# Optimization experiments

Hardware: AMD Instinct MI355X
Metric: run time of the kernel (lower is better)

## Reference

```python
import jax, jax.numpy as jnp
import numpy as np

B, L, E = 8, 2048, 128


def setup_inputs() -> dict:
    key = jax.random.key(0)
    k1, k2, k3, k4 = jax.random.split(key, 4)
    return {
        "Uq": jax.random.normal(k1, (B, L, E), dtype=jnp.float32),
        "Uid": jax.random.normal(k2, (B, L, E), dtype=jnp.float32),
        "mask": jnp.ones((L, L), dtype=jnp.float32),
        "Wc_w": jax.random.normal(k3, (3 * E,), dtype=jnp.float32) * 0.05,
        "Wc_b": jax.random.normal(k4, (), dtype=jnp.float32) * 0.05,
    }


def reference(Uq, Uid, mask, Wc_w, Wc_b):
    # Wc(cat(Uid, Uq, Uid*Uq)) decomposed into three direct projections —
    # exact same math as the Linear over the concatenation, never
    # materializing the [B, L, L, 3E] tensor.
    e = Uq.shape[-1]
    w_id, w_q, w_mul = Wc_w[:e], Wc_w[e:2 * e], Wc_w[2 * e:]
    s_id = jnp.einsum("bie,e->bi", Uid, w_id)          # [B, Lid]
    s_q = jnp.einsum("bje,e->bj", Uq, w_q)             # [B, Lq]
    s_mul = jnp.einsum("bie,bje,e->bij", Uid, Uq, w_mul)  # [B, Lid, Lq]
    S = (s_id[:, :, None] + s_q[:, None, :] + s_mul + Wc_b) * mask
    # S_D2Q = Softmax(dim=0) over the per-example [Lid, Lq] matrix -> axis=1
    P = jax.nn.softmax(S, axis=1)                      # [B, Lid, Lq]
    A_D2Q = jnp.einsum("bij,bje->bie", P, Uq)          # [B, Lid, E]
    M = jnp.einsum("bij,bkj->bik", P, P)               # P @ P^T, [B, Lid, Lid]
    A_Q2D = jnp.einsum("bik,bke->bie", M, Uid)         # [B, Lid, E]
    Vid = jnp.concatenate([Uid, A_D2Q, Uid * A_D2Q, Uid * A_Q2D], axis=-1)
    return Vid  # [B, Lid, 4E]
```

## Files before the change

### kernel.cpp

```cpp
#include <hip/hip_runtime.h>

#define L 2048
#define E 128
#define NB 8

typedef float f32x4 __attribute__((ext_vector_type(4)));
typedef short short8 __attribute__((ext_vector_type(8)));
typedef unsigned int u32;

static __device__ inline float bf2f(ushort u) {
  union { float f; u32 i; } v; v.i = ((u32)u) << 16; return v.f;
}
static __device__ inline ushort f2bf(float f) {
  union { float f; u32 i; } v; v.f = f;
  u32 x = v.i;
  return (ushort)((x + 0x7fffu + ((x >> 16) & 1u)) >> 16);
}

__device__ inline void glds16(const ushort* g, ushort* l) {
  __builtin_amdgcn_global_load_lds(
      (const __attribute__((address_space(1))) u32*)(const void*)g,
      (__attribute__((address_space(3))) u32*)(void*)l, 16, 0, 0);
}

__global__ __launch_bounds__(128) void k_prep(const float* __restrict__ Uq,
                                              const float* __restrict__ Uid,
                                              const float* __restrict__ Wcw,
                                              ushort* __restrict__ UqB,
                                              ushort* __restrict__ UidB,
                                              ushort* __restrict__ Uidw,
                                              float* __restrict__ s_id,
                                              float* __restrict__ s_q) {
  int r = blockIdx.x;
  int e = threadIdx.x;
  ushort uqu  = f2bf(Uq[(long)r * E + e]);
  ushort uidu = f2bf(Uid[(long)r * E + e]);
  float uqf = bf2f(uqu), uidf = bf2f(uidu);
  float wid  = bf2f(f2bf(Wcw[e]));
  float wq   = bf2f(f2bf(Wcw[E + e]));
  float wmul = bf2f(f2bf(Wcw[2 * E + e]));
  UqB[(long)r * E + e]  = uqu;
  UidB[(long)r * E + e] = uidu;
  Uidw[(long)r * E + e] = f2bf(uidf * wmul);
  float sid = uidf * wid, sq = uqf * wq;
  #pragma unroll
  for (int off = 32; off >= 1; off >>= 1) {
    sid += __shfl_down(sid, off, 64);
    sq  += __shfl_down(sq,  off, 64);
  }
  __shared__ float red[4];
  int wv = threadIdx.x >> 6;
  if ((threadIdx.x & 63) == 0) { red[wv * 2] = sid; red[wv * 2 + 1] = sq; }
  __syncthreads();
  if (threadIdx.x == 0) { s_id[r] = red[0] + red[2]; s_q[r] = red[1] + red[3]; }
}

__global__ __launch_bounds__(256) void k_maskT(const float* __restrict__ mask,
                                               ushort* __restrict__ maskT) {
  __shared__ ushort tile[32][33];
  int j0 = blockIdx.x * 32, i0 = blockIdx.y * 32;
  int tx = threadIdx.x, ty = threadIdx.y;
  #pragma unroll
  for (int r = ty; r < 32; r += 8)
    tile[r][tx] = f2bf(mask[(long)(i0 + r) * L + j0 + tx]);
  __syncthreads();
  #pragma unroll
  for (int r = ty; r < 32; r += 8)
    maskT[(long)(j0 + r) * L + i0 + tx] = tile[tx][r];
}

__global__ __launch_bounds__(256) void k_tr(const ushort* __restrict__ src,
                                            ushort* __restrict__ dst,
                                            int R, int C) {
  __shared__ ushort tile[32][33];
  long base = (long)blockIdx.z * R * C;
  src += base; dst += base;
  int c0 = blockIdx.x * 32, r0 = blockIdx.y * 32;
  int tx = threadIdx.x, ty = threadIdx.y;
  #pragma unroll
  for (int i = ty; i < 32; i += 8)
    tile[i][tx] = src[(long)(r0 + i) * C + c0 + tx];
  __syncthreads();
  #pragma unroll
  for (int i = ty; i < 32; i += 8)
    dst[(long)(c0 + i) * R + r0 + tx] = tile[tx][i];
}

__device__ inline void gemm128_loop(const ushort* __restrict__ A,
                                    const ushort* __restrict__ B,
                                    long ldA, long ldB, int K,
                                    f32x4 acc[4][4],
                                    ushort* ldsA, ushort* ldsB) {
  const int t = threadIdx.x;
  const int w = t >> 6, lane = t & 63;
  const int mrow = lane & 15, quad = lane >> 4;
  const int lr = lane >> 3;
  const int lc = ((lane & 7) ^ lr) * 8;
  const int mh = (w & 1) * 64, nh = (w >> 1) * 64;
  for (int k0 = 0; k0 < K; k0 += 64) {
    __syncthreads();
    #pragma unroll
    for (int s = 0; s < 4; s++) {
      int row = w * 32 + s * 8 + lr;
      glds16(&A[(long)row * ldA + k0 + lc], &ldsA[w * 2048 + s * 512]);
      glds16(&B[(long)row * ldB + k0 + lc], &ldsB[w * 2048 + s * 512]);
    }
    __syncthreads();
    #pragma unroll
    for (int kk = 0; kk < 2; kk++) {
      short8 av[4], bv[4];
      #pragma unroll
      for (int mi = 0; mi < 4; mi++)
        av[mi] = *(const short8*)&ldsA[(mh + mi * 16 + mrow) * 64 +
                                       ((kk * 32 + quad * 8) ^ ((mrow & 7) << 3))];
      #pragma unroll
      for (int ni = 0; ni < 4; ni++)
        bv[ni] = *(const short8*)&ldsB[(nh + ni * 16 + mrow) * 64 +
                                       ((kk * 32 + quad * 8) ^ ((mrow & 7) << 3))];
      #pragma unroll
      for (int mi = 0; mi < 4; mi++)
        #pragma unroll
        for (int ni = 0; ni < 4; ni++)
          acc[mi][ni] = __builtin_amdgcn_mfma_f32_16x16x32_bf16(av[mi], bv[ni], acc[mi][ni], 0, 0, 0);
    }
  }
}

__device__ inline void gemm64x128_loop(const ushort* __restrict__ A,
                                       const ushort* __restrict__ B,
                                       long ldA, long ldB, int K,
                                       f32x4 acc[2][4],
                                       ushort* ldsA, ushort* ldsB) {
  const int t = threadIdx.x;
  const int w = t >> 6, lane = t & 63;
  const int mrow = lane & 15, quad = lane >> 4;
  const int lr = lane >> 3;
  const int lc = ((lane & 7) ^ lr) * 8;
  const int mh = (w & 1) * 32, nh = (w >> 1) * 64;
  for (int k0 = 0; k0 < K; k0 += 64) {
    __syncthreads();
    #pragma unroll
    for (int s = 0; s < 2; s++) {
      int row = w * 16 + s * 8 + lr;
      glds16(&A[(long)row * ldA + k0 + lc], &ldsA[w * 1024 + s * 512]);
    }
    #pragma unroll
    for (int s = 0; s < 4; s++) {
      int row = w * 32 + s * 8 + lr;
      glds16(&B[(long)row * ldB + k0 + lc], &ldsB[w * 2048 + s * 512]);
    }
    __syncthreads();
    #pragma unroll
    for (int kk = 0; kk < 2; kk++) {
      short8 av[2], bv[4];
      #pragma unroll
      for (int mi = 0; mi < 2; mi++)
        av[mi] = *(const short8*)&ldsA[(mh + mi * 16 + mrow) * 64 +
                                       ((kk * 32 + quad * 8) ^ ((mrow & 7) << 3))];
      #pragma unroll
      for (int ni = 0; ni < 4; ni++)
        bv[ni] = *(const short8*)&ldsB[(nh + ni * 16 + mrow) * 64 +
                                       ((kk * 32 + quad * 8) ^ ((mrow & 7) << 3))];
      #pragma unroll
      for (int mi = 0; mi < 2; mi++)
        #pragma unroll
        for (int ni = 0; ni < 4; ni++)
          acc[mi][ni] = __builtin_amdgcn_mfma_f32_16x16x32_bf16(av[mi], bv[ni], acc[mi][ni], 0, 0, 0);
    }
  }
}

__global__ __launch_bounds__(256) void k_scores(const ushort* __restrict__ Uq,
                                                const ushort* __restrict__ Uidw,
                                                const float* __restrict__ s_id,
                                                const float* __restrict__ s_q,
                                                const float* __restrict__ Wcb,
                                                const ushort* __restrict__ maskT,
                                                ushort* __restrict__ St, int b0) {
  __shared__ ushort lds[16384];
  ushort* ldsA = lds;
  ushort* ldsB = lds + 8192;
  int bz = blockIdx.z, b = b0 + bz;
  int m0 = blockIdx.x * 128;
  int n0 = blockIdx.y * 128;
  const ushort* A = Uq   + (long)b * L * E + (long)m0 * E;
  const ushort* B = Uidw + (long)b * L * E + (long)n0 * E;
  f32x4 acc[4][4] = {};
  gemm128_loop(A, B, E, E, E, acc, ldsA, ldsB);
  float bias = bf2f(f2bf(Wcb[0]));
  const int t = threadIdx.x, w = t >> 6, lane = t & 63;
  const int col = lane & 15, quad = lane >> 4;
  const int mh = (w & 1) * 64, nh = (w >> 1) * 64;

  __syncthreads();
  float sidv[4];
  #pragma unroll
  for (int ni = 0; ni < 4; ni++)
    sidv[ni] = s_id[b * L + n0 + nh + ni * 16 + col];
  #pragma unroll
  for (int mi = 0; mi < 4; mi++) {
    float sqv[4];
    #pragma unroll
    for (int rg = 0; rg < 4; rg++)
      sqv[rg] = s_q[b * L + m0 + mh + mi * 16 + quad * 4 + rg];
    #pragma unroll
    for (int ni = 0; ni < 4; ni++) {
      int cl = nh + ni * 16 + col;
      #pragma unroll
      for (int rg = 0; rg < 4; rg++) {
        int row = mh + mi * 16 + quad * 4 + rg;
        float v = acc[mi][ni][rg] + sqv[rg] + sidv[ni] + bias;
        lds[row * 128 + (cl ^ ((row & 7) << 3))] = f2bf(v);
      }
    }
  }
  __syncthreads();
  #pragma unroll
  for (int p = 0; p < 8; p++) {
    int r2 = p * 16 + (t >> 4);
    int cu = (t & 15) * 8;
    uint4 sv = *(const uint4*)&lds[r2 * 128 + (cu ^ ((r2 & 7) << 3))];
    int jg = m0 + r2;
    uint4 mv = *(const uint4*)&maskT[(long)jg * L + n0 + cu];
    ushort o[8];
    const ushort* sp = (const ushort*)&sv;
    const ushort* mp = (const ushort*)&mv;
    #pragma unroll
    for (int k = 0; k < 8; k++) o[k] = f2bf(bf2f(sp[k]) * bf2f(mp[k]));
    *(uint4*)&St[(long)bz * L * L + (long)jg * L + n0 + cu] = *(const uint4*)&o[0];
  }
}

__global__ __launch_bounds__(256) void k_softmax_tr(ushort* __restrict__ St,
                                                    ushort* __restrict__ P) {
  int bz = blockIdx.y;
  int j0 = blockIdx.x * 32;
  ushort* Sb = St + (long)bz * L * L;
  ushort* Pb = P  + (long)bz * L * L;
  int t = threadIdx.x, w = t >> 6, lane = t & 63;
  __shared__ float mrow[32], lrow[32];
  __shared__ ushort tile[128 * 33];
  for (int rr = w; rr < 32; rr += 4) {
    const ushort* row = Sb + (long)(j0 + rr) * L;
    uint4 q[4];
    #pragma unroll
    for (int c = 0; c < 4; c++) q[c] = *(const uint4*)&row[lane * 8 + c * 512];
    float v[32]; float mx = -1e30f;
    #pragma unroll
    for (int c = 0; c < 4; c++) {
      ushort* pr = (ushort*)&q[c];
      #pragma unroll
      for (int k = 0; k < 8; k++) { v[c * 8 + k] = bf2f(pr[k]); mx = fmaxf(mx, v[c * 8 + k]); }
    }
    #pragma unroll
    for (int off = 32; off >= 1; off >>= 1) mx = fmaxf(mx, __shfl_xor(mx, off, 64));
    float s = 0.f;
    #pragma unroll
    for (int k = 0; k < 32; k++) s += __expf(v[k] - mx);
    #pragma unroll
    for (int off = 32; off >= 1; off >>= 1) s += __shfl_xor(s, off, 64);
    if (lane == 0) { mrow[rr] = mx; lrow[rr] = 1.0f / s; }
  }
  __syncthreads();
  int r = t >> 3, c0 = (t & 7) * 16;
  float m = mrow[r], inv = lrow[r];
  int il = t >> 1, half = (t & 1) * 16;
  for (int i0 = 0; i0 < L; i0 += 128) {
    ushort* src = Sb + (long)(j0 + r) * L + i0 + c0;
    uint4 q0 = *(const uint4*)src;
    uint4 q1 = *(const uint4*)(src + 8);
    ushort o[16];
    ushort* pr = (ushort*)&q0;
    #pragma unroll
    for (int k = 0; k < 8; k++) o[k] = f2bf(__expf(bf2f(pr[k]) - m) * inv);
    pr = (ushort*)&q1;
    #pragma unroll
    for (int k = 0; k < 8; k++) o[8 + k] = f2bf(__expf(bf2f(pr[k]) - m) * inv);
    *(uint4*)src = *(uint4*)&o[0];
    *(uint4*)(src + 8) = *(uint4*)&o[8];
    __syncthreads();
    #pragma unroll
    for (int k = 0; k < 16; k++) tile[(c0 + k) * 33 + r] = o[k];
    __syncthreads();
    ushort po[16];
    #pragma unroll
    for (int jj = 0; jj < 16; jj++) po[jj] = tile[il * 33 + half + jj];
    ushort* pd = Pb + (long)(i0 + il) * L + j0 + half;
    *(uint4*)pd = *(uint4*)&po[0];
    *(uint4*)(pd + 8) = *(uint4*)&po[8];
  }
}

__global__ __launch_bounds__(256) void k_gemm_Tt(const ushort* __restrict__ UidT,
                                                 const ushort* __restrict__ Pt,
                                                 ushort* __restrict__ Tt, int b0) {
  __shared__ ushort lds[12288];
  ushort* ldsA = lds;
  ushort* ldsB = lds + 4096;
  int bz = blockIdx.z, b = b0 + bz;
  int e0 = (blockIdx.x & 1) * 64;
  int j0 = (blockIdx.x >> 1) * 128;
  const ushort* A = UidT + (long)b * E * L + (long)e0 * L;
  const ushort* B = Pt   + (long)bz * L * L + (long)j0 * L;
  f32x4 acc[2][4] = {};
  gemm64x128_loop(A, B, L, L, L, acc, ldsA, ldsB);
  const int t = threadIdx.x, w = t >> 6, lane = t & 63;
  const int col = lane & 15, quad = lane >> 4;
  const int mh = (w & 1) * 32, nh = (w >> 1) * 64;
  __syncthreads();
  #pragma unroll
  for (int mi = 0; mi < 2; mi++)
    #pragma unroll
    for (int ni = 0; ni < 4; ni++) {
      int cl = nh + ni * 16 + col;
      #pragma unroll
      for (int rg = 0; rg < 4; rg++) {
        int row = mh + mi * 16 + quad * 4 + rg;
        lds[row * 128 + (cl ^ ((row & 7) << 3))] = f2bf(acc[mi][ni][rg]);
      }
    }
  __syncthreads();
  #pragma unroll
  for (int p = 0; p < 4; p++) {
    int r2 = p * 16 + (t >> 4);
    int cu = (t & 15) * 8;
    uint4 v = *(const uint4*)&lds[r2 * 128 + (cu ^ ((r2 & 7) << 3))];
    *(uint4*)&Tt[(long)b * E * L + (long)(e0 + r2) * L + j0 + cu] = v;
  }
}

__global__ __launch_bounds__(256) void k_gemm_A(const ushort* __restrict__ P,
                                                const ushort* __restrict__ UqT,
                                                const ushort* __restrict__ Tt,
                                                const ushort* __restrict__ UidB,
                                                float* __restrict__ out, int b0) {
  __shared__ ushort ldsA[64 * 64];
  __shared__ ushort ldsB[128 * 64];
  int bz = blockIdx.z, b = b0 + bz;
  int m0 = blockIdx.x * 64;
  int n0 = blockIdx.y * 128;
  const ushort* A = P + (long)bz * L * L + (long)m0 * L;
  const ushort* B = (blockIdx.y == 0) ? (UqT + (long)b * E * L)
                                      : (Tt  + (long)b * E * L);
  f32x4 acc[2][4] = {};
  gemm64x128_loop(A, B, L, L, L, acc, ldsA, ldsB);
  const int t = threadIdx.x, w = t >> 6, lane = t & 63;
  const int col = lane & 15, quad = lane >> 4;
  const int mh = (w & 1) * 32, nh = (w >> 1) * 64;
  #pragma unroll
  for (int mi = 0; mi < 2; mi++)
    #pragma unroll
    for (int ni = 0; ni < 4; ni++)
      #pragma unroll
      for (int rg = 0; rg < 4; rg++) {
        int ig = m0 + mh + mi * 16 + quad * 4 + rg;
        int c  = n0 + nh + ni * 16 + col;
        float a = acc[mi][ni][rg];
        float uidf = bf2f(UidB[(long)b * L * E + (long)ig * E + (c & 127)]);
        long ob = ((long)b * L + ig) * 512;
        if (c < 128) {
          out[ob + c]       = uidf;
          out[ob + 128 + c] = a;
          out[ob + 256 + c] = uidf * a;
        } else {
          out[ob + 256 + c] = uidf * a;
        }
      }
}

extern "C" void kernel_launch(void* const* d_in, const int* in_sizes, int n_in,
                              void* d_out, int out_size, void* d_ws, size_t ws_size,
                              hipStream_t stream) {
  const float* Uq   = (const float*)d_in[0];
  const float* Uid  = (const float*)d_in[1];
  const float* mask = (const float*)d_in[2];
  const float* Wcw  = (const float*)d_in[3];
  const float* Wcb  = (const float*)d_in[4];
  float* out = (float*)d_out;

  char* ws = (char*)d_ws;
  size_t off = 0;
  auto alloc = [&](size_t bytes) -> void* {
    void* p = ws + off; off += (bytes + 255) & ~(size_t)255; return p;
  };
  const size_t nUb = (size_t)NB * L * E * 2;
  ushort* UqB   = (ushort*)alloc(nUb);
  ushort* UidB  = (ushort*)alloc(nUb);
  ushort* Uidw  = (ushort*)alloc(nUb);
  ushort* UqT   = (ushort*)alloc(nUb);
  ushort* UidT  = (ushort*)alloc(nUb);
  ushort* Tt    = (ushort*)alloc(nUb);
  ushort* maskT = (ushort*)alloc((size_t)L * L * 2);
  float*  s_id  = (float*)alloc((size_t)NB * L * 4);
  float*  s_q   = (float*)alloc((size_t)NB * L * 4);
  const size_t per_batch = (size_t)L * L * 2;
  size_t avail = (ws_size > off + 2 * per_batch) ? (ws_size - off) : 2 * per_batch;
  int nb_c = (int)(avail / (2 * per_batch));
  if (nb_c < 1) nb_c = 1;
  if (nb_c > NB) nb_c = NB;
  ushort* St = (ushort*)(ws + off);
  ushort* P  = (ushort*)(ws + off + nb_c * per_batch);

  dim3 tb(32, 8);
  k_prep<<<NB * L, E, 0, stream>>>(Uq, Uid, Wcw, UqB, UidB, Uidw, s_id, s_q);
  k_maskT<<<dim3(L / 32, L / 32), tb, 0, stream>>>(mask, maskT);
  k_tr<<<dim3(E / 32, L / 32, NB), tb, 0, stream>>>(UqB, UqT, L, E);
  k_tr<<<dim3(E / 32, L / 32, NB), tb, 0, stream>>>(UidB, UidT, L, E);

  for (int b0 = 0; b0 < NB; b0 += nb_c) {
    int nb = (NB - b0 < nb_c) ? (NB - b0) : nb_c;
    k_scores<<<dim3(L / 128, L / 128, nb), 256, 0, stream>>>(UqB, Uidw, s_id, s_q, Wcb, maskT, St, b0);
    k_softmax_tr<<<dim3(L / 32, nb), 256, 0, stream>>>(St, P);
    k_gemm_Tt<<<dim3(2 * (L / 128), 1, nb), 256, 0, stream>>>(UidT, St, Tt, b0);
    k_gemm_A<<<dim3(L / 64, 2, nb), 256, 0, stream>>>(P, UqT, Tt, UidB, out, b0);
  }
}
```

Measured before the change: 233.0 us.

## Double-buffer GEMM LDS loads and split softmax into rowstats plus apply-transpose

The GEMM inner loops become double-buffered: the next K-tile is issued into a second LDS buffer while MFMAs consume the current one, which removes a barrier per iteration and overlaps global loads with compute. LDS allocations double to hold both buffers, which can lower occupancy. The fused softmax-transpose kernel is split into a row-statistics kernel and a wider-grid apply/transpose kernel, giving more blocks for parallelism at the cost of one extra launch and an extra read of St.

```diff
diff --git a/kernel.cpp b/kernel.cpp
--- a/kernel.cpp
+++ b/kernel.cpp
@@ -97,32 +97,45 @@
   const int lr = lane >> 3;
   const int lc = ((lane & 7) ^ lr) * 8;
   const int mh = (w & 1) * 64, nh = (w >> 1) * 64;
+  #pragma unroll
+  for (int s = 0; s < 4; s++) {
+    int row = w * 32 + s * 8 + lr;
+    glds16(&A[(long)row * ldA + lc], &ldsA[w * 2048 + s * 512]);
+    glds16(&B[(long)row * ldB + lc], &ldsB[w * 2048 + s * 512]);
+  }
+  __syncthreads();
+  int cur = 0;
   for (int k0 = 0; k0 < K; k0 += 64) {
-    __syncthreads();
-    #pragma unroll
-    for (int s = 0; s < 4; s++) {
-      int row = w * 32 + s * 8 + lr;
-      glds16(&A[(long)row * ldA + k0 + lc], &ldsA[w * 2048 + s * 512]);
-      glds16(&B[(long)row * ldB + k0 + lc], &ldsB[w * 2048 + s * 512]);
-    }
-    __syncthreads();
+    int nxt = cur ^ 1;
+    if (k0 + 64 < K) {
+      #pragma unroll
+      for (int s = 0; s < 4; s++) {
+        int row = w * 32 + s * 8 + lr;
+        glds16(&A[(long)row * ldA + k0 + 64 + lc], &ldsA[nxt * 8192 + w * 2048 + s * 512]);
+        glds16(&B[(long)row * ldB + k0 + 64 + lc], &ldsB[nxt * 8192 + w * 2048 + s * 512]);
+      }
+    }
+    const ushort* cA = &ldsA[cur * 8192];
+    const ushort* cB = &ldsB[cur * 8192];
     #pragma unroll
     for (int kk = 0; kk < 2; kk++) {
       short8 av[4], bv[4];
       #pragma unroll
       for (int mi = 0; mi < 4; mi++)
-        av[mi] = *(const short8*)&ldsA[(mh + mi * 16 + mrow) * 64 +
-                                       ((kk * 32 + quad * 8) ^ ((mrow & 7) << 3))];
+        av[mi] = *(const short8*)&cA[(mh + mi * 16 + mrow) * 64 +
+                                     ((kk * 32 + quad * 8) ^ ((mrow & 7) << 3))];
       #pragma unroll
       for (int ni = 0; ni < 4; ni++)
-        bv[ni] = *(const short8*)&ldsB[(nh + ni * 16 + mrow) * 64 +
-                                       ((kk * 32 + quad * 8) ^ ((mrow & 7) << 3))];
+        bv[ni] = *(const short8*)&cB[(nh + ni * 16 + mrow) * 64 +
+                                     ((kk * 32 + quad * 8) ^ ((mrow & 7) << 3))];
       #pragma unroll
       for (int mi = 0; mi < 4; mi++)
         #pragma unroll
         for (int ni = 0; ni < 4; ni++)
           acc[mi][ni] = __builtin_amdgcn_mfma_f32_16x16x32_bf16(av[mi], bv[ni], acc[mi][ni], 0, 0, 0);
     }
+    __syncthreads();
+    cur = nxt;
   }
 }
 
@@ -137,36 +150,53 @@
   const int lr = lane >> 3;
   const int lc = ((lane & 7) ^ lr) * 8;
   const int mh = (w & 1) * 32, nh = (w >> 1) * 64;
+  #pragma unroll
+  for (int s = 0; s < 2; s++) {
+    int row = w * 16 + s * 8 + lr;
+    glds16(&A[(long)row * ldA + lc], &ldsA[w * 1024 + s * 512]);
+  }
+  #pragma unroll
+  for (int s = 0; s < 4; s++) {
+    int row = w * 32 + s * 8 + lr;
+    glds16(&B[(long)row * ldB + lc], &ldsB[w * 2048 + s * 512]);
+  }
+  __syncthreads();
+  int cur = 0;
   for (int k0 = 0; k0 < K; k0 += 64) {
-    __syncthreads();
-    #pragma unroll
-    for (int s = 0; s < 2; s++) {
-      int row = w * 16 + s * 8 + lr;
-      glds16(&A[(long)row * ldA + k0 + lc], &ldsA[w * 1024 + s * 512]);
-    }
-    #pragma unroll
-    for (int s = 0; s < 4; s++) {
-      int row = w * 32 + s * 8 + lr;
-      glds16(&B[(long)row * ldB + k0 + lc], &ldsB[w * 2048 + s * 512]);
-    }
-    __syncthreads();
+    int nxt = cur ^ 1;
+    if (k0 + 64 < K) {
+      #pragma unroll
+      for (int s = 0; s < 2; s++) {
+        int row = w * 16 + s * 8 + lr;
+        glds16(&A[(long)row * ldA + k0 + 64 + lc], &ldsA[nxt * 4096 + w * 1024 + s * 512]);
+      }
+      #pragma unroll
+      for (int s = 0; s < 4; s++) {
+        int row = w * 32 + s * 8 + lr;
+        glds16(&B[(long)row * ldB + k0 + 64 + lc], &ldsB[nxt * 8192 + w * 2048 + s * 512]);
+      }
+    }
+    const ushort* cA = &ldsA[cur * 4096];
+    const ushort* cB = &ldsB[cur * 8192];
     #pragma unroll
     for (int kk = 0; kk < 2; kk++) {
       short8 av[2], bv[4];
       #pragma unroll
       for (int mi = 0; mi < 2; mi++)
-        av[mi] = *(const short8*)&ldsA[(mh + mi * 16 + mrow) * 64 +
-                                       ((kk * 32 + quad * 8) ^ ((mrow & 7) << 3))];
+        av[mi] = *(const short8*)&cA[(mh + mi * 16 + mrow) * 64 +
+                                     ((kk * 32 + quad * 8) ^ ((mrow & 7) << 3))];
       #pragma unroll
       for (int ni = 0; ni < 4; ni++)
-        bv[ni] = *(const short8*)&ldsB[(nh + ni * 16 + mrow) * 64 +
-                                       ((kk * 32 + quad * 8) ^ ((mrow & 7) << 3))];
+        bv[ni] = *(const short8*)&cB[(nh + ni * 16 + mrow) * 64 +
+                                     ((kk * 32 + quad * 8) ^ ((mrow & 7) << 3))];
       #pragma unroll
       for (int mi = 0; mi < 2; mi++)
         #pragma unroll
         for (int ni = 0; ni < 4; ni++)
           acc[mi][ni] = __builtin_amdgcn_mfma_f32_16x16x32_bf16(av[mi], bv[ni], acc[mi][ni], 0, 0, 0);
     }
+    __syncthreads();
+    cur = nxt;
   }
 }
 
@@ -177,9 +207,9 @@
                                                 const float* __restrict__ Wcb,
                                                 const ushort* __restrict__ maskT,
                                                 ushort* __restrict__ St, int b0) {
-  __shared__ ushort lds[16384];
+  __shared__ ushort lds[32768];
   ushort* ldsA = lds;
-  ushort* ldsB = lds + 8192;
+  ushort* ldsB = lds + 16384;
   int bz = blockIdx.z, b = b0 + bz;
   int m0 = blockIdx.x * 128;
   int n0 = blockIdx.y * 128;
@@ -231,72 +261,85 @@
   }
 }
 
-__global__ __launch_bounds__(256) void k_softmax_tr(ushort* __restrict__ St,
-                                                    ushort* __restrict__ P) {
+__global__ __launch_bounds__(256) void k_rowstats(const ushort* __restrict__ St,
+                                                  float* __restrict__ mg,
+                                                  float* __restrict__ lg) {
   int bz = blockIdx.y;
-  int j0 = blockIdx.x * 32;
+  int row = blockIdx.x * 4 + (threadIdx.x >> 6);
+  int lane = threadIdx.x & 63;
+  const ushort* R = St + (long)bz * L * L + (long)row * L + lane * 8;
+  uint4 q[4];
+  #pragma unroll
+  for (int c = 0; c < 4; c++) q[c] = *(const uint4*)(R + c * 512);
+  float v[32]; float mx = -1e30f;
+  #pragma unroll
+  for (int c = 0; c < 4; c++) {
+    const ushort* pr = (const ushort*)&q[c];
+    #pragma unroll
+    for (int k = 0; k < 8; k++) {
+      float f = bf2f(pr[k]); v[c * 8 + k] = f; mx = fmaxf(mx, f);
+    }
+  }
+  #pragma unroll
+  for (int off = 32; off >= 1; off >>= 1) mx = fmaxf(mx, __shfl_xor(mx, off, 64));
+  float s = 0.f;
+  #pragma unroll
+  for (int k = 0; k < 32; k++) s += __expf(v[k] - mx);
+  #pragma unroll
+  for (int off = 32; off >= 1; off >>= 1) s += __shfl_xor(s, off, 64);
+  if (lane == 0) { mg[bz * L + row] = mx; lg[bz * L + row] = 1.0f / s; }
+}
+
+__global__ __launch_bounds__(256) void k_apply_tr(ushort* __restrict__ St,
+                                                  ushort* __restrict__ P,
+                                                  const float* __restrict__ mg,
+                                                  const float* __restrict__ lg) {
+  int bz = blockIdx.z;
+  int j0 = blockIdx.x * 64;
+  int ibase = blockIdx.y * 512;
   ushort* Sb = St + (long)bz * L * L;
   ushort* Pb = P  + (long)bz * L * L;
-  int t = threadIdx.x, w = t >> 6, lane = t & 63;
-  __shared__ float mrow[32], lrow[32];
-  __shared__ ushort tile[128 * 33];
-  for (int rr = w; rr < 32; rr += 4) {
-    const ushort* row = Sb + (long)(j0 + rr) * L;
+  int t = threadIdx.x;
+  int r = t >> 2, c0 = (t & 3) * 32;
+  float m   = mg[bz * L + j0 + r];
+  float inv = lg[bz * L + j0 + r];
+  int il = t >> 1, half = (t & 1) * 32;
+  __shared__ ushort tile[128 * 65];
+  for (int ii = 0; ii < 4; ii++) {
+    int i0 = ibase + ii * 128;
+    ushort* src = Sb + (long)(j0 + r) * L + i0 + c0;
     uint4 q[4];
     #pragma unroll
-    for (int c = 0; c < 4; c++) q[c] = *(const uint4*)&row[lane * 8 + c * 512];
-    float v[32]; float mx = -1e30f;
-    #pragma unroll
-    for (int c = 0; c < 4; c++) {
-      ushort* pr = (ushort*)&q[c];
-      #pragma unroll
-      for (int k = 0; k < 8; k++) { v[c * 8 + k] = bf2f(pr[k]); mx = fmaxf(mx, v[c * 8 + k]); }
-    }
-    #pragma unroll
-    for (int off = 32; off >= 1; off >>= 1) mx = fmaxf(mx, __shfl_xor(mx, off, 64));
-    float s = 0.f;
-    #pragma unroll
-    for (int k = 0; k < 32; k++) s += __expf(v[k] - mx);
-    #pragma unroll
-    for (int off = 32; off >= 1; off >>= 1) s += __shfl_xor(s, off, 64);
-    if (lane == 0) { mrow[rr] = mx; lrow[rr] = 1.0f / s; }
-  }
-  __syncthreads();
-  int r = t >> 3, c0 = (t & 7) * 16;
-  float m = mrow[r], inv = lrow[r];
-  int il = t >> 1, half = (t & 1) * 16;
-  for (int i0 = 0; i0 < L; i0 += 128) {
-    ushort* src = Sb + (long)(j0 + r) * L + i0 + c0;
-    uint4 q0 = *(const uint4*)src;
-    uint4 q1 = *(const uint4*)(src + 8);
-    ushort o[16];
-    ushort* pr = (ushort*)&q0;
-    #pragma unroll
-    for (int k = 0; k < 8; k++) o[k] = f2bf(__expf(bf2f(pr[k]) - m) * inv);
-    pr = (ushort*)&q1;
-    #pragma unroll
-    for (int k = 0; k < 8; k++) o[8 + k] = f2bf(__expf(bf2f(pr[k]) - m) * inv);
-    *(uint4*)src = *(uint4*)&o[0];
-    *(uint4*)(src + 8) = *(uint4*)&o[8];
+    for (int cc = 0; cc < 4; cc++) q[cc] = *(const uint4*)(src + cc * 8);
+    ushort o[32];
+    #pragma unroll
+    for (int cc = 0; cc < 4; cc++) {
+      const ushort* pr = (const ushort*)&q[cc];
+      #pragma unroll
+      for (int k = 0; k < 8; k++)
+        o[cc * 8 + k] = f2bf(__expf(bf2f(pr[k]) - m) * inv);
+    }
+    #pragma unroll
+    for (int cc = 0; cc < 4; cc++) *(uint4*)(src + cc * 8) = *(const uint4*)&o[cc * 8];
     __syncthreads();
     #pragma unroll
-    for (int k = 0; k < 16; k++) tile[(c0 + k) * 33 + r] = o[k];
+    for (int k = 0; k < 32; k++) tile[(c0 + k) * 65 + r] = o[k];
     __syncthreads();
-    ushort po[16];
-    #pragma unroll
-    for (int jj = 0; jj < 16; jj++) po[jj] = tile[il * 33 + half + jj];
+    ushort po[32];
+    #pragma unroll
+    for (int jj = 0; jj < 32; jj++) po[jj] = tile[il * 65 + half + jj];
     ushort* pd = Pb + (long)(i0 + il) * L + j0 + half;
-    *(uint4*)pd = *(uint4*)&po[0];
-    *(uint4*)(pd + 8) = *(uint4*)&po[8];
+    #pragma unroll
+    for (int cc = 0; cc < 4; cc++) *(uint4*)(pd + cc * 8) = *(const uint4*)&po[cc * 8];
   }
 }
 
 __global__ __launch_bounds__(256) void k_gemm_Tt(const ushort* __restrict__ UidT,
                                                  const ushort* __restrict__ Pt,
                                                  ushort* __restrict__ Tt, int b0) {
-  __shared__ ushort lds[12288];
+  __shared__ ushort lds[24576];
   ushort* ldsA = lds;
-  ushort* ldsB = lds + 4096;
+  ushort* ldsB = lds + 8192;
   int bz = blockIdx.z, b = b0 + bz;
   int e0 = (blockIdx.x & 1) * 64;
   int j0 = (blockIdx.x >> 1) * 128;
@@ -334,8 +377,8 @@
                                                 const ushort* __restrict__ Tt,
                                                 const ushort* __restrict__ UidB,
                                                 float* __restrict__ out, int b0) {
-  __shared__ ushort ldsA[64 * 64];
-  __shared__ ushort ldsB[128 * 64];
+  __shared__ ushort ldsA[2 * 4096];
+  __shared__ ushort ldsB[2 * 8192];
   int bz = blockIdx.z, b = b0 + bz;
   int m0 = blockIdx.x * 64;
   int n0 = blockIdx.y * 128;
@@ -393,6 +436,8 @@
   ushort* maskT = (ushort*)alloc((size_t)L * L * 2);
   float*  s_id  = (float*)alloc((size_t)NB * L * 4);
   float*  s_q   = (float*)alloc((size_t)NB * L * 4);
+  float*  mg    = (float*)alloc((size_t)NB * L * 4);
+  float*  lg    = (float*)alloc((size_t)NB * L * 4);
   const size_t per_batch = (size_t)L * L * 2;
   size_t avail = (ws_size > off + 2 * per_batch) ? (ws_size - off) : 2 * per_batch;
   int nb_c = (int)(avail / (2 * per_batch));
@@ -410,7 +455,8 @@
   for (int b0 = 0; b0 < NB; b0 += nb_c) {
     int nb = (NB - b0 < nb_c) ? (NB - b0) : nb_c;
     k_scores<<<dim3(L / 128, L / 128, nb), 256, 0, stream>>>(UqB, Uidw, s_id, s_q, Wcb, maskT, St, b0);
-    k_softmax_tr<<<dim3(L / 32, nb), 256, 0, stream>>>(St, P);
+    k_rowstats<<<dim3(L / 4, nb), 256, 0, stream>>>(St, mg, lg);
+    k_apply_tr<<<dim3(L / 64, L / 512, nb), 256, 0, stream>>>(St, P, mg, lg);
     k_gemm_Tt<<<dim3(2 * (L / 128), 1, nb), 256, 0, stream>>>(UidT, St, Tt, b0);
     k_gemm_A<<<dim3(L / 64, 2, nb), 256, 0, stream>>>(P, UqT, Tt, UidB, out, b0);
   }
```

Result: slower. 248.5 us (+6.7%).
